# Kernel optimization log

Measured on AMD Instinct MI355X. Metric: run time of the kernel, lower is better.

Reference implementation:

```python
import jax, jax.numpy as jnp
import numpy as np

OUT_K = 7  # out_kernel


def setup_inputs() -> dict:
    key = jax.random.key(0)
    k = jax.random.split(key, 12)
    b, cin, h, w = 2, 256, 64, 64
    C, pd = 64, 4          # out_channels, pos_dim
    qc = C - pd            # channels produced by conv_q/k/v
    s = 0.05
    f32 = jnp.float32
    return {
        "x":    jax.random.normal(k[0], (b, cin, h, w), f32),
        "Wq":   jax.random.normal(k[1], (qc, cin), f32) * s,
        "bq":   jax.random.normal(k[2], (qc,), f32) * s,
        "Wk":   jax.random.normal(k[3], (qc, cin), f32) * s,
        "bk":   jax.random.normal(k[4], (qc,), f32) * s,
        "Wv":   jax.random.normal(k[5], (qc, cin), f32) * s,
        "bv":   jax.random.normal(k[6], (qc,), f32) * s,
        "Wp":   jax.random.normal(k[7], (pd, 2), f32) * s,
        "bp":   jax.random.normal(k[8], (pd,), f32) * s,
        "Wout": jax.random.normal(k[9], (C, C, OUT_K, OUT_K), f32) * s,
        "bout": jax.random.normal(k[10], (C,), f32) * s,
    }


def reference(x, Wq, bq, Wk, bk, Wv, bv, Wp, bp, Wout, bout):
    b, cin, h, w = x.shape
    C = Wout.shape[0]  # out_channels
    dt = x.dtype

    # positional encoding: hw_pose is (row_index, col_index) grids -> 1x1 conv to pos_dim chans
    rows = jnp.broadcast_to(jnp.arange(h, dtype=dt)[:, None], (h, w))
    cols = jnp.broadcast_to(jnp.arange(w, dtype=dt)[None, :], (h, w))
    grid = jnp.stack([rows, cols], axis=0)                      # (2,h,w)
    pos = jnp.einsum('oc,chw->ohw', Wp, grid) + bp[:, None, None]  # (pd,h,w)
    pos = jnp.broadcast_to(pos[None], (b,) + pos.shape)         # (b,pd,h,w)

    def conv1x1(W, bias):
        return jnp.einsum('bchw,oc->bohw', x, W) + bias[None, :, None, None]

    qs = jnp.concatenate([conv1x1(Wq, bq), pos], axis=1)        # (b,C,h,w)
    ks = jnp.concatenate([conv1x1(Wk, bk), pos], axis=1)
    vs = jnp.concatenate([conv1x1(Wv, bv), pos], axis=1)

    hw = h * w
    qsf = qs.transpose(0, 2, 3, 1).reshape(b, hw, C)            # (b,hw,C)
    ksf = ks.reshape(b, C, hw)                                  # (b,C,hw)
    vsf = vs.transpose(0, 2, 3, 1)                              # (b,h,w,C)

    qk = jnp.einsum('bnc,bcm->bnm', qsf, ksf) / jnp.sqrt(jnp.asarray(C, dt))
    diag = jnp.arange(hw)
    qk = qk.at[:, diag, diag].set(0.0)                          # zero diagonal BEFORE softmax
    attn = jax.nn.softmax(qk, axis=-1).reshape(b, h, w, h, w)

    # 7x7 clamped neighborhood gather (replaces the 49-iteration python loop)
    r = OUT_K // 2
    offs = jnp.arange(-r, r + 1)
    hi = jnp.clip(jnp.arange(h)[:, None] + offs[None, :], 0, h - 1)  # (h,7)
    wi = jnp.clip(jnp.arange(w)[:, None] + offs[None, :], 0, w - 1)  # (w,7)
    ii = jnp.arange(h)[:, None, None, None]
    jj = jnp.arange(w)[None, :, None, None]
    hk = hi[:, None, :, None]
    wk = wi[None, :, None, :]
    attn_loc = attn[:, ii, jj, hk, wk]                          # (b,h,w,7,7)
    v_loc = vsf[:, hk, wk, :]                                   # (b,h,w,7,7,C)

    qkv = attn_loc[..., None] * v_loc                           # (b,h,w,7,7,C)
    # con_out: kernel=7, stride=7 over a 7x7 patch == full contraction
    out = jnp.einsum('bhwklc,ockl->bhwo', qkv, Wout) + bout     # (b,h,w,C)
    out = jax.nn.relu(out)
    return out.transpose(0, 3, 1, 2)                            # (b,C,h,w)
```

## Files before the change

kernel.cpp:

```cpp
#include <hip/hip_runtime.h>
#include <math.h>

#define NTAP 49

typedef short bf16x8 __attribute__((ext_vector_type(8)));
typedef float f32x4  __attribute__((ext_vector_type(4)));

__device__ __forceinline__ float b2f(ushort u) {
    return __uint_as_float(((unsigned)u) << 16);
}
__device__ __forceinline__ ushort f2b(float f) {
    unsigned u = __float_as_uint(f);
    return (ushort)((u + 0x7FFFu + ((u >> 16) & 1u)) >> 16);
}
__device__ __forceinline__ int iclamp(int x) { return min(max(x, 0), 63); }

#define LOG2E 1.44269504f
#define S2    (0.125f * LOG2E)

#define WTB_OFF 0u
#define QH_OFF  598016u
#define KH_OFF  1646592u
#define VH_OFF  2695168u
#define LP_OFF  3743744u
#define MXQ_OFF 4005888u
#define MXK_OFF 4006912u

__device__ __forceinline__ float mh_reduce(const float* __restrict__ MXq,
                                           const float* __restrict__ MXk,
                                           int b, int t, float* sh) {
    if (t < 64) {
        float a = fmaxf(MXq[(b << 7) + t], MXq[(b << 7) + 64 + t]);
        float k = fmaxf(MXk[(b << 7) + t], MXk[(b << 7) + 64 + t]);
        #pragma unroll
        for (int off = 1; off < 64; off <<= 1) {
            a = fmaxf(a, __shfl_xor(a, off, 64));
            k = fmaxf(k, __shfl_xor(k, off, 64));
        }
        if (t == 0) *sh = 0.125f * sqrtf(a) * sqrtf(k) + 1.0f;
    }
    __syncthreads();
    return *sh;
}

__global__ __launch_bounds__(512, 2) void k_qkv(
    const float* __restrict__ x,
    const float* __restrict__ Wq, const float* __restrict__ Wk, const float* __restrict__ Wv,
    const float* __restrict__ bq, const float* __restrict__ bk, const float* __restrict__ bv,
    const float* __restrict__ Wp, const float* __restrict__ bp,
    ushort* __restrict__ QKV, float* __restrict__ MXq, float* __restrict__ MXk)
{
    __shared__ ushort Xh[32 * 256];
    __shared__ ushort Xl[32 * 256];
    __shared__ ushort Wshl[192 * 64];
    __shared__ float  sqL[64];
    int bid0 = blockIdx.x;
    int bid  = (bid0 & 7) * 32 + (bid0 >> 3);
    int b   = bid >> 7;
    int n0  = (bid & 127) * 32;
    int t   = threadIdx.x;
    int w    = t >> 6;
    int L    = t & 63;
    int lrow = L & 15, lk = L >> 4;

    if (t < 64) sqL[t] = 0.f;
    {
        int p  = t & 31;
        int cg = t >> 5;
        #pragma unroll
        for (int it = 0; it < 2; ++it) {
            int cgi = cg + it * 16;
            float v[8];
            #pragma unroll
            for (int e = 0; e < 8; ++e)
                v[e] = x[((size_t)(b * 256 + cgi * 8 + e) << 12) + n0 + p];
            bf16x8 hi, lo;
            #pragma unroll
            for (int e = 0; e < 8; ++e) {
                ushort h = f2b(v[e]);
                hi[e] = (short)h;
                lo[e] = (short)f2b(v[e] - b2f(h));
            }
            int off = p * 256 + ((cgi * 8) ^ ((p & 7) * 8));
            *(bf16x8*)(Xh + off) = hi;
            *(bf16x8*)(Xl + off) = lo;
        }
    }

    int   s_och[3], s_g[3];
    bool  s_live[3];
    const float* s_src[3];
    #pragma unroll
    for (int s = 0; s < 3; ++s) {
        int g_idx = t + s * 512;
        int och = g_idx >> 3, g = g_idx & 7;
        int mat = och >> 6, o = och & 63;
        const float* Wm = (mat == 0) ? Wq : (mat == 1) ? Wk : Wv;
        s_och[s] = och; s_g[s] = g;
        s_live[s] = (o < 60);
        s_src[s] = Wm + o * 256 + (g & 3) * 8;
    }
    float4 wreg[3][2];

    #define ISSUE_W(c8) {                                                   \
        _Pragma("unroll")                                                   \
        for (int s = 0; s < 3; ++s) {                                       \
            if (s_live[s]) {                                                \
                const float* sp = s_src[s] + (c8) * 32;                     \
                wreg[s][0] = *(const float4*)(sp);                          \
                wreg[s][1] = *(const float4*)(sp + 4);                      \
            } else {                                                        \
                wreg[s][0] = make_float4(0.f,0.f,0.f,0.f);                  \
                wreg[s][1] = make_float4(0.f,0.f,0.f,0.f);                  \
            }                                                               \
        } }
    #define WRITE_W() {                                                     \
        _Pragma("unroll")                                                   \
        for (int s = 0; s < 3; ++s) {                                       \
            float vv[8] = {wreg[s][0].x, wreg[s][0].y, wreg[s][0].z,        \
                           wreg[s][0].w, wreg[s][1].x, wreg[s][1].y,        \
                           wreg[s][1].z, wreg[s][1].w};                     \
            bf16x8 val;                                                     \
            _Pragma("unroll")                                               \
            for (int e = 0; e < 8; ++e) {                                   \
                ushort h = f2b(vv[e]);                                      \
                val[e] = (s_g[s] < 4) ? (short)h                            \
                                      : (short)f2b(vv[e] - b2f(h));         \
            }                                                               \
            *(bf16x8*)((char*)Wshl + s_och[s] * 128 +                       \
                       ((s_g[s] * 16) ^ ((s_och[s] & 7) << 4))) = val;      \
        } }

    ISSUE_W(0);
    __syncthreads();
    WRITE_W();
    __syncthreads();

    int pxh = w >> 2;
    int ob  = (w & 3) * 48;
    int px  = pxh * 16 + lrow;

    f32x4 acc[3] = {{0,0,0,0},{0,0,0,0},{0,0,0,0}};

    for (int c8 = 0; c8 < 8; ++c8) {
        if (c8 + 1 < 8) ISSUE_W(c8 + 1);
        int cidx = (c8 * 4 + lk) * 8;
        int o0 = px * 256 + (cidx ^ ((px & 7) * 8));
        bf16x8 ah = *(const bf16x8*)(Xh + o0);
        bf16x8 al = *(const bf16x8*)(Xl + o0);
        #pragma unroll
        for (int c = 0; c < 3; ++c) {
            int och = ob + c * 16 + lrow;
            const char* wb = (const char*)Wshl + och * 128;
            int swz = (och & 7) << 4;
            bf16x8 bh = *(const bf16x8*)(wb + ((lk * 16) ^ swz));
            bf16x8 bl = *(const bf16x8*)(wb + (((4 + lk) * 16) ^ swz));
            acc[c] = __builtin_amdgcn_mfma_f32_16x16x32_bf16(al, bh, acc[c], 0, 0, 0);
            acc[c] = __builtin_amdgcn_mfma_f32_16x16x32_bf16(ah, bl, acc[c], 0, 0, 0);
            acc[c] = __builtin_amdgcn_mfma_f32_16x16x32_bf16(ah, bh, acc[c], 0, 0, 0);
        }
        __syncthreads();
        if (c8 + 1 < 8) WRITE_W();
        __syncthreads();
    }

    float s_q[4] = {0,0,0,0}, s_k[4] = {0,0,0,0};
    #pragma unroll
    for (int c = 0; c < 3; ++c) {
        int och = ob + c * 16 + lrow;
        int mat = och >> 6;
        int o   = och & 63;
        const float* bm = (mat == 0) ? bq : (mat == 1) ? bk : bv;
        ushort* Ob = QKV + (size_t)mat * 524288;
        if (o < 60) {
            float bias = bm[o];
            #pragma unroll
            for (int e = 0; e < 4; ++e) {
                int n = n0 + pxh * 16 + lk * 4 + e;
                float v = acc[c][e] + bias;
                Ob[((size_t)((b << 12) + n)) * 64 + o] = f2b(v);
                if (mat == 0) s_q[e] = fmaf(v, v, s_q[e]);
                else if (mat == 1) s_k[e] = fmaf(v, v, s_k[e]);
            }
        } else {
            int po = o - 60;
            float w0 = Wp[2 * po], w1 = Wp[2 * po + 1], b0 = bp[po];
            #pragma unroll
            for (int e = 0; e < 4; ++e) {
                int n = n0 + pxh * 16 + lk * 4 + e;
                float fi = (float)(n >> 6), fj = (float)(n & 63);
                float pv = fmaf(w0, fi, fmaf(w1, fj, b0));
                Ob[((size_t)((b << 12) + n)) * 64 + o] = f2b(pv);
                if (mat == 0) s_q[e] = fmaf(pv, pv, s_q[e]);
                else if (mat == 1) s_k[e] = fmaf(pv, pv, s_k[e]);
            }
        }
    }
    #pragma unroll
    for (int off = 1; off < 16; off <<= 1) {
        #pragma unroll
        for (int e = 0; e < 4; ++e) {
            s_q[e] += __shfl_xor(s_q[e], off, 64);
            s_k[e] += __shfl_xor(s_k[e], off, 64);
        }
    }
    if (lrow == 0) {
        #pragma unroll
        for (int e = 0; e < 4; ++e) {
            int pix = pxh * 16 + lk * 4 + e;
            atomicAdd(&sqL[pix],      s_q[e]);
            atomicAdd(&sqL[32 + pix], s_k[e]);
        }
    }
    __syncthreads();
    if (t < 32) {
        float q2 = sqL[t], k2 = sqL[32 + t];
        #pragma unroll
        for (int off = 1; off < 32; off <<= 1) {
            q2 = fmaxf(q2, __shfl_xor(q2, off, 64));
            k2 = fmaxf(k2, __shfl_xor(k2, off, 64));
        }
        if (t == 0) { MXq[bid] = q2; MXk[bid] = k2; }
    }
}

__global__ __launch_bounds__(512, 2) void k_stats(
    const float* __restrict__ Wout, ushort* __restrict__ Wtb,
    const ushort* __restrict__ QH, const ushort* __restrict__ KH,
    const float* __restrict__ MXq, const float* __restrict__ MXk,
    float* __restrict__ Lp)
{
    __shared__ ushort Ks[2][128 * 64];
    __shared__ float  mhs;
    int bid0 = blockIdx.x;
    int bid  = (bid0 & 7) * 64 + (bid0 >> 3);
    int ks  = bid & 7;
    int r   = bid >> 3;
    int b   = r >> 5;
    int n0  = (r & 31) * 128;
    int ck0 = ks * 512;
    int t = threadIdx.x;

    {
        int widx = bid * 512 + t;
        if (widx < 64 * 64 * NTAP) {
            int o   = widx / (64 * NTAP);
            int rem = widx - o * (64 * NTAP);
            int c   = rem / NTAP;
            int kl  = rem - c * NTAP;
            Wtb[(o * NTAP + kl) * 64 + c] = f2b(Wout[widx]);
        }
    }
    float bse = -mh_reduce(MXq, MXk, b, t, &mhs) * LOG2E;

    int w = t >> 6, L = t & 63;
    int lrow = L & 15, lk = L >> 4;

    size_t qbase = ((size_t)((b << 12) + n0 + w * 16 + lrow)) * 64 + lk * 8;
    bf16x8 a0 = *(const bf16x8*)(QH + qbase);
    bf16x8 a1 = *(const bf16x8*)(QH + qbase + 32);

    #pragma unroll
    for (int gi = 0; gi < 2; ++gi) {
        int g = t + gi * 512;
        int u = g >> 3, c8 = g & 7;
        bf16x8 val = *(const bf16x8*)(KH + ((size_t)((b << 12) + ck0 + u)) * 64 + c8 * 8);
        *(bf16x8*)((char*)Ks[0] + u * 128 + ((c8 * 16) ^ ((u & 7) << 4))) = val;
    }

    float rs0 = 0.f, rs1 = 0.f, rs2 = 0.f, rs3 = 0.f;

    for (int c = 0; c < 4; ++c) {
        bf16x8 st0, st1;
        int u0 = t >> 3, c80 = t & 7;
        int u1 = (t + 512) >> 3, c81 = t & 7;
        bool pf = (c + 1) < 4;
        if (pf) {
            st0 = *(const bf16x8*)(KH + ((size_t)((b << 12) + ck0 + (c + 1) * 128 + u0)) * 64 + c80 * 8);
            st1 = *(const bf16x8*)(KH + ((size_t)((b << 12) + ck0 + (c + 1) * 128 + u1)) * 64 + c81 * 8);
        }
        __syncthreads();
        const char* kb = (const char*)Ks[c & 1];
        #pragma unroll
        for (int kg = 0; kg < 8; ++kg) {
            int u = kg * 16 + lrow;
            int swz = (u & 7) << 4;
            bf16x8 b0 = *(const bf16x8*)(kb + u * 128 + ((lk * 16) ^ swz));
            bf16x8 b1 = *(const bf16x8*)(kb + u * 128 + ((64 + lk * 16) ^ swz));
            f32x4 z = {0.f, 0.f, 0.f, 0.f};
            z = __builtin_amdgcn_mfma_f32_16x16x32_bf16(a0, b0, z, 0, 0, 0);
            z = __builtin_amdgcn_mfma_f32_16x16x32_bf16(a1, b1, z, 0, 0, 0);
            rs0 += exp2f(fmaf(z[0], S2, bse));
            rs1 += exp2f(fmaf(z[1], S2, bse));
            rs2 += exp2f(fmaf(z[2], S2, bse));
            rs3 += exp2f(fmaf(z[3], S2, bse));
        }
        if (pf) {
            char* kn = (char*)Ks[(c + 1) & 1];
            *(bf16x8*)(kn + u0 * 128 + ((c80 * 16) ^ ((u0 & 7) << 4))) = st0;
            *(bf16x8*)(kn + u1 * 128 + ((c81 * 16) ^ ((u1 & 7) << 4))) = st1;
        }
    }
    #pragma unroll
    for (int off = 1; off < 16; off <<= 1) {
        rs0 += __shfl_xor(rs0, off, 64);
        rs1 += __shfl_xor(rs1, off, 64);
        rs2 += __shfl_xor(rs2, off, 64);
        rs3 += __shfl_xor(rs3, off, 64);
    }
    if (lrow == 0) {
        float* dst = Lp + ((size_t)(ks * 2 + b) << 12) + n0 + w * 16 + lk * 4;
        dst[0] = rs0; dst[1] = rs1; dst[2] = rs2; dst[3] = rs3;
    }
}

__global__ __launch_bounds__(512, 1) void k_out(
    const ushort* __restrict__ QH, const ushort* __restrict__ KH,
    const ushort* __restrict__ VH, const ushort* __restrict__ Wtb,
    const float* __restrict__ Lp,
    const float* __restrict__ MXq, const float* __restrict__ MXk,
    const float* __restrict__ bout, float* __restrict__ out)
{
    __shared__ ushort Vs[7 * 40 * 64];
    __shared__ ushort Kh[7 * 40 * 64];
    __shared__ ushort Ws[7 * 64 * 64];
    __shared__ float  Al2[NTAP * 36];
    __shared__ float  Lrow[32];
    __shared__ float  LcS[32];
    __shared__ float  mhs;
    int bid0 = blockIdx.x;
    int bid  = (bid0 & 7) * 32 + (bid0 >> 3);
    int b   = bid >> 7;
    int rem = bid & 127;
    int i   = rem >> 1;
    int j0  = (rem & 1) * 32;
    int n0  = (i << 6) + j0;
    int t   = threadIdx.x;
    int w    = t >> 6;
    int L    = t & 63;
    int lrow = L & 15, lk = L >> 4;

    float bse = -mh_reduce(MXq, MXk, b, t, &mhs) * LOG2E;
    float e0  = exp2f(bse);

    bf16x8 wreg[7];
    #define ISSUE_WS(kk) {                                                          \
        _Pragma("unroll")                                                           \
        for (int s = 0; s < 7; ++s) {                                               \
            int g = t + s * 512;                                                    \
            int c8 = g & 7, och = (g >> 3) & 63, ll = g >> 9;                       \
            wreg[s] = *(const bf16x8*)(Wtb + ((size_t)(och * NTAP + (kk) * 7 + ll)) * 64 + c8 * 8); \
        } }
    #define WRITE_WS() {                                                            \
        _Pragma("unroll")                                                           \
        for (int s = 0; s < 7; ++s) {                                               \
            int g = t + s * 512;                                                    \
            int c8 = g & 7, och = (g >> 3) & 63, ll = g >> 9;                       \
            *(bf16x8*)((char*)Ws + ll * 8192 + och * 128 +                          \
                       ((c8 * 16) ^ ((och & 7) << 4))) = wreg[s];                   \
        } }

    for (int g = t; g < 2 * 7 * 38 * 8; g += 512) {
        int which = g >= 7 * 38 * 8;
        int gg = which ? g - 7 * 38 * 8 : g;
        int kk = gg / 304;
        int r2 = gg - kk * 304;
        int u  = r2 >> 3, c8 = r2 & 7;
        int vr = iclamp(i + kk - 3);
        int vc = iclamp(j0 - 3 + u);
        const ushort* src = which ? KH : VH;
        ushort* dst = which ? Kh : Vs;
        bf16x8 val = *(const bf16x8*)(src + ((size_t)((b << 12) + (vr << 6) + vc)) * 64 + c8 * 8);
        *(bf16x8*)((char*)dst + kk * 5120 + u * 128 + ((c8 * 16) ^ ((u & 7) << 4))) = val;
    }
    ISSUE_WS(0);
    WRITE_WS();
    if (t < 32) {
        int n = n0 + t;
        float s = 0.f;
        #pragma unroll
        for (int ks = 0; ks < 8; ++ks)
            s += Lp[((size_t)(ks * 2 + b) << 12) + n];
        Lrow[t] = s;
    }
    __syncthreads();

    {
        int p = t >> 4, u = t & 15;
        int n = n0 + p;
        int pj = n & 63;
        const ushort* qr = QH + ((size_t)(b << 12) + n) * 64;
        bf16x8 qv[8];
        #pragma unroll
        for (int c8 = 0; c8 < 8; ++c8) qv[c8] = *(const bf16x8*)(qr + c8 * 8);

        int nt = (u == 0) ? 4 : 3;
        float d[4] = {0.f, 0.f, 0.f, 0.f};
        int srcs[4];
        const char* kbp[4];
        int swzs[4];
        #pragma unroll
        for (int m = 0; m < 4; ++m) {
            int tap = (m == 3) ? 48 : (u + 16 * m);
            int kk = tap / 7, ll = tap - kk * 7;
            srcs[m] = (iclamp(i + kk - 3) << 6) + iclamp(pj + ll - 3);
            int uu = p + ll;
            kbp[m]  = (const char*)Kh + kk * 5120 + uu * 128;
            swzs[m] = (uu & 7) << 4;
        }
        #pragma unroll
        for (int c8 = 0; c8 < 8; ++c8) {
            bf16x8 kv0 = *(const bf16x8*)(kbp[0] + ((c8 * 16) ^ swzs[0]));
            bf16x8 kv1 = *(const bf16x8*)(kbp[1] + ((c8 * 16) ^ swzs[1]));
            bf16x8 kv2 = *(const bf16x8*)(kbp[2] + ((c8 * 16) ^ swzs[2]));
            #pragma unroll
            for (int e = 0; e < 8; ++e) {
                float q = b2f((ushort)qv[c8][e]);
                d[0] = fmaf(q, b2f((ushort)kv0[e]), d[0]);
                d[1] = fmaf(q, b2f((ushort)kv1[e]), d[1]);
                d[2] = fmaf(q, b2f((ushort)kv2[e]), d[2]);
            }
        }
        if (nt == 4) {
            #pragma unroll
            for (int c8 = 0; c8 < 8; ++c8) {
                bf16x8 kv3 = *(const bf16x8*)(kbp[3] + ((c8 * 16) ^ swzs[3]));
                #pragma unroll
                for (int e = 0; e < 8; ++e)
                    d[3] = fmaf(b2f((ushort)qv[c8][e]), b2f((ushort)kv3[e]), d[3]);
            }
        }
        if (u == 8)
            LcS[p] = Lrow[p] - exp2f(fmaf(d[1], S2, bse)) + e0;
        __syncthreads();
        float rLc = 1.0f / LcS[p];
        for (int m = 0; m < nt; ++m) {
            int tap = (m == 3) ? 48 : (u + 16 * m);
            float A = (srcs[m] == n) ? (e0 * rLc)
                                     : (exp2f(fmaf(d[m], S2, bse)) * rLc);
            Al2[tap * 36 + p] = A;
        }
    }
    __syncthreads();

    int q16 = (w >> 2) << 4;
    int o16 = (w & 3) << 4;
    int oA  = o16 + lrow;
    int wswz = (oA & 7) << 4;
    f32x4 acc0 = {0.f, 0.f, 0.f, 0.f};

    for (int kk = 0; kk < 7; ++kk) {
        if (kk + 1 < 7) ISSUE_WS(kk + 1);
        const char* vrow = (const char*)Vs + kk * 5120;
        #pragma unroll
        for (int ll = 0; ll < 7; ++ll) {
            int kl = kk * 7 + ll;
            int u = q16 + lrow + ll;
            const char* vb = vrow + u * 128;
            int swz = (u & 7) << 4;
            bf16x8 v0 = *(const bf16x8*)(vb + ((lk * 16) ^ swz));
            bf16x8 v1 = *(const bf16x8*)(vb + ((64 + lk * 16) ^ swz));
            float4 av = *(const float4*)(&Al2[kl * 36 + q16 + lk * 4]);
            const char* wb = (const char*)Ws + ll * 8192 + oA * 128;
            bf16x8 b00 = *(const bf16x8*)(wb + ((lk * 16) ^ wswz));
            bf16x8 b01 = *(const bf16x8*)(wb + (((4 + lk) * 16) ^ wswz));
            f32x4 z = {0.f, 0.f, 0.f, 0.f};
            z = __builtin_amdgcn_mfma_f32_16x16x32_bf16(v0, b00, z, 0, 0, 0);
            z = __builtin_amdgcn_mfma_f32_16x16x32_bf16(v1, b01, z, 0, 0, 0);
            acc0[0] = fmaf(av.x, z[0], acc0[0]);
            acc0[1] = fmaf(av.y, z[1], acc0[1]);
            acc0[2] = fmaf(av.z, z[2], acc0[2]);
            acc0[3] = fmaf(av.w, z[3], acc0[3]);
        }
        __syncthreads();
        if (kk + 1 < 7) WRITE_WS();
        __syncthreads();
    }

    int o = oA;
    int nbase = n0 + q16 + lk * 4;
    float bb = bout[o];
    float4 v = make_float4(fmaxf(acc0[0] + bb, 0.f), fmaxf(acc0[1] + bb, 0.f),
                           fmaxf(acc0[2] + bb, 0.f), fmaxf(acc0[3] + bb, 0.f));
    *(float4*)(out + (((size_t)(b * 64 + o)) << 12) + nbase) = v;
}

extern "C" void kernel_launch(void* const* d_in, const int* in_sizes, int n_in,
                              void* d_out, int out_size, void* d_ws, size_t ws_size,
                              hipStream_t stream) {
    const float* x    = (const float*)d_in[0];
    const float* Wq   = (const float*)d_in[1];
    const float* bq   = (const float*)d_in[2];
    const float* Wk   = (const float*)d_in[3];
    const float* bk   = (const float*)d_in[4];
    const float* Wv   = (const float*)d_in[5];
    const float* bv   = (const float*)d_in[6];
    const float* Wp   = (const float*)d_in[7];
    const float* bp   = (const float*)d_in[8];
    const float* Wout = (const float*)d_in[9];
    const float* bout = (const float*)d_in[10];
    float* out = (float*)d_out;

    char* ws = (char*)d_ws;
    ushort* Wtb = (ushort*)(ws + WTB_OFF);
    ushort* QKV = (ushort*)(ws + QH_OFF);
    float*  Lp  = (float*)(ws + LP_OFF);
    float*  MXq = (float*)(ws + MXQ_OFF);
    float*  MXk = (float*)(ws + MXK_OFF);

    ushort* QH = QKV;
    ushort* KH = QKV + 524288;
    ushort* VH = QKV + 1048576;

    hipLaunchKernelGGL(k_qkv,   dim3(256), dim3(512), 0, stream,
                       x, Wq, Wk, Wv, bq, bk, bv, Wp, bp, QKV, MXq, MXk);
    hipLaunchKernelGGL(k_stats, dim3(512), dim3(512), 0, stream,
                       Wout, Wtb, QH, KH, MXq, MXk, Lp);
    hipLaunchKernelGGL(k_out,   dim3(256), dim3(512), 0, stream,
                       QH, KH, VH, Wtb, Lp, MXq, MXk, bout, out);
}
```

Baseline: 46.64 us.

## Split 7x7 output-conv taps across wave pairs, widen per-wave channel tile, reduce via LDS

Each wave now computes 32 output channels, two 16x16 MFMA tiles sharing the V operand, instead of 16. The waves are split into two parity groups that take alternating ll taps, with the assignment flipping each kk row. The two groups' partial sums are combined through shared memory before the bias, ReLU and store. The aim is to reuse V fragment loads across two B tiles and to balance the tap work. The cost is an extra LDS reduction and barrier, more accumulator registers, and an uneven 4/3 tap split per row.

```diff
diff --git a/kernel.cpp b/kernel.cpp
--- a/kernel.cpp
+++ b/kernel.cpp
@@ -443,46 +443,83 @@
     }
     __syncthreads();
 
-    int q16 = (w >> 2) << 4;
-    int o16 = (w & 3) << 4;
-    int oA  = o16 + lrow;
-    int wswz = (oA & 7) << 4;
+    int par = w >> 2;
+    int sub = w & 3;
+    int q16 = (sub >> 1) << 4;
+    int o32 = (sub & 1) << 5;
+    int oA0 = o32 + lrow;
+    int oA1 = o32 + 16 + lrow;
+    int wswz = (oA0 & 7) << 4;
     f32x4 acc0 = {0.f, 0.f, 0.f, 0.f};
+    f32x4 acc1 = {0.f, 0.f, 0.f, 0.f};
 
     for (int kk = 0; kk < 7; ++kk) {
         if (kk + 1 < 7) ISSUE_WS(kk + 1);
         const char* vrow = (const char*)Vs + kk * 5120;
-        #pragma unroll
-        for (int ll = 0; ll < 7; ++ll) {
-            int kl = kk * 7 + ll;
-            int u = q16 + lrow + ll;
-            const char* vb = vrow + u * 128;
-            int swz = (u & 7) << 4;
-            bf16x8 v0 = *(const bf16x8*)(vb + ((lk * 16) ^ swz));
-            bf16x8 v1 = *(const bf16x8*)(vb + ((64 + lk * 16) ^ swz));
-            float4 av = *(const float4*)(&Al2[kl * 36 + q16 + lk * 4]);
-            const char* wb = (const char*)Ws + ll * 8192 + oA * 128;
-            bf16x8 b00 = *(const bf16x8*)(wb + ((lk * 16) ^ wswz));
-            bf16x8 b01 = *(const bf16x8*)(wb + (((4 + lk) * 16) ^ wswz));
-            f32x4 z = {0.f, 0.f, 0.f, 0.f};
-            z = __builtin_amdgcn_mfma_f32_16x16x32_bf16(v0, b00, z, 0, 0, 0);
-            z = __builtin_amdgcn_mfma_f32_16x16x32_bf16(v1, b01, z, 0, 0, 0);
-            acc0[0] = fmaf(av.x, z[0], acc0[0]);
-            acc0[1] = fmaf(av.y, z[1], acc0[1]);
-            acc0[2] = fmaf(av.z, z[2], acc0[2]);
-            acc0[3] = fmaf(av.w, z[3], acc0[3]);
+        int ll0 = par ^ (kk & 1);
+        #pragma unroll
+        for (int l2 = 0; l2 < 4; ++l2) {
+            int ll = ll0 + 2 * l2;
+            if (ll < 7) {
+                int kl = kk * 7 + ll;
+                int u = q16 + lrow + ll;
+                const char* vb = vrow + u * 128;
+                int swz = (u & 7) << 4;
+                bf16x8 v0 = *(const bf16x8*)(vb + ((lk * 16) ^ swz));
+                bf16x8 v1 = *(const bf16x8*)(vb + ((64 + lk * 16) ^ swz));
+                float4 av = *(const float4*)(&Al2[kl * 36 + q16 + lk * 4]);
+                const char* wb0 = (const char*)Ws + ll * 8192 + oA0 * 128;
+                const char* wb1 = (const char*)Ws + ll * 8192 + oA1 * 128;
+                bf16x8 b00 = *(const bf16x8*)(wb0 + ((lk * 16) ^ wswz));
+                bf16x8 b01 = *(const bf16x8*)(wb0 + (((4 + lk) * 16) ^ wswz));
+                bf16x8 b10 = *(const bf16x8*)(wb1 + ((lk * 16) ^ wswz));
+                bf16x8 b11 = *(const bf16x8*)(wb1 + (((4 + lk) * 16) ^ wswz));
+                f32x4 z = {0.f, 0.f, 0.f, 0.f};
+                z = __builtin_amdgcn_mfma_f32_16x16x32_bf16(v0, b00, z, 0, 0, 0);
+                z = __builtin_amdgcn_mfma_f32_16x16x32_bf16(v1, b01, z, 0, 0, 0);
+                f32x4 y = {0.f, 0.f, 0.f, 0.f};
+                y = __builtin_amdgcn_mfma_f32_16x16x32_bf16(v0, b10, y, 0, 0, 0);
+                y = __builtin_amdgcn_mfma_f32_16x16x32_bf16(v1, b11, y, 0, 0, 0);
+                acc0[0] = fmaf(av.x, z[0], acc0[0]);
+                acc0[1] = fmaf(av.y, z[1], acc0[1]);
+                acc0[2] = fmaf(av.z, z[2], acc0[2]);
+                acc0[3] = fmaf(av.w, z[3], acc0[3]);
+                acc1[0] = fmaf(av.x, y[0], acc1[0]);
+                acc1[1] = fmaf(av.y, y[1], acc1[1]);
+                acc1[2] = fmaf(av.z, y[2], acc1[2]);
+                acc1[3] = fmaf(av.w, y[3], acc1[3]);
+            }
         }
         __syncthreads();
         if (kk + 1 < 7) WRITE_WS();
         __syncthreads();
     }
 
-    int o = oA;
-    int nbase = n0 + q16 + lk * 4;
-    float bb = bout[o];
-    float4 v = make_float4(fmaxf(acc0[0] + bb, 0.f), fmaxf(acc0[1] + bb, 0.f),
-                           fmaxf(acc0[2] + bb, 0.f), fmaxf(acc0[3] + bb, 0.f));
-    *(float4*)(out + (((size_t)(b * 64 + o)) << 12) + nbase) = v;
+    {
+        float* S = (float*)Kh;
+        if (par == 1) {
+            *(f32x4*)(S + (sub * 2 + 0) * 256 + L * 4) = acc0;
+            *(f32x4*)(S + (sub * 2 + 1) * 256 + L * 4) = acc1;
+        }
+        __syncthreads();
+        if (par == 0) {
+            f32x4 p0 = *(const f32x4*)(S + (sub * 2 + 0) * 256 + L * 4);
+            f32x4 p1 = *(const f32x4*)(S + (sub * 2 + 1) * 256 + L * 4);
+            int nbase = n0 + q16 + lk * 4;
+            float bb0 = bout[oA0];
+            float bb1 = bout[oA1];
+            float4 v0 = make_float4(fmaxf(acc0[0] + p0[0] + bb0, 0.f),
+                                    fmaxf(acc0[1] + p0[1] + bb0, 0.f),
+                                    fmaxf(acc0[2] + p0[2] + bb0, 0.f),
+                                    fmaxf(acc0[3] + p0[3] + bb0, 0.f));
+            float4 v1 = make_float4(fmaxf(acc1[0] + p1[0] + bb1, 0.f),
+                                    fmaxf(acc1[1] + p1[1] + bb1, 0.f),
+                                    fmaxf(acc1[2] + p1[2] + bb1, 0.f),
+                                    fmaxf(acc1[3] + p1[3] + bb1, 0.f));
+            *(float4*)(out + (((size_t)(b * 64 + oA0)) << 12) + nbase) = v0;
+            *(float4*)(out + (((size_t)(b * 64 + oA1)) << 12) + nbase) = v1;
+        }
+    }
 }
 
 extern "C" void kernel_launch(void* const* d_in, const int* in_sizes, int n_in,
```

Result: slower. 50.41 us (+8.1%).
